# Optimization experiments

Measured on AMD Instinct MI355X. Metric: run time of the kernel, lower is better.

Reference implementation:

```python
import jax, jax.numpy as jnp
import numpy as np

TAU = 0.1          # temperature from init_kwargs
EPS = 1e-8         # torch.nn.CosineSimilarity default eps


def setup_inputs() -> dict:
    key = jax.random.key(0)
    k1, k2, k3 = jax.random.split(key, 3)
    B, D = 2048, 128
    return {
        "z_i": jax.random.normal(k1, (B, D), dtype=jnp.float32),
        "z_j": jax.random.normal(k2, (B, D), dtype=jnp.float32),
        "y": jax.random.randint(k3, (B,), 0, 10, dtype=jnp.int64),
    }


def reference(z_i, z_j, y):
    # p: (2N, D)
    p = jnp.concatenate([z_i, z_j], axis=0)
    n2 = p.shape[0]
    # Cosine similarity via norms + single GEMM (same math as pairwise
    # CosineSimilarity: dot / max(||a||*||b||, eps)), then temperature scale.
    norms = jnp.linalg.norm(p, axis=1)                      # (2N,)
    sim = (p @ p.T) / jnp.maximum(norms[:, None] * norms[None, :], EPS) / TAU

    # Positive mask: same label, diagonal removed.
    y2 = jnp.concatenate([y, y], axis=0)                    # (2N,)
    off_diag = 1.0 - jnp.eye(n2, dtype=sim.dtype)           # logit mask
    mask = (y2[:, None] == y2[None, :]).astype(sim.dtype) * off_diag

    # Masked log-softmax over each row (self excluded from denominator).
    exp_logits = jnp.exp(sim) * off_diag
    log_prob = sim - jnp.log(exp_logits.sum(axis=1, keepdims=True))

    mean_log_prob_pos = (mask * log_prob).sum(axis=1) / mask.sum(axis=1)
    return -mean_log_prob_pos.mean()
```

## Files before the change

kernel.cpp:

```cpp
#include <hip/hip_runtime.h>

#define N2 4096
#define D 128
#define TAU_INV 10.0f
#define E2SCALE 14.4269504088896340736f
#define BM 256
#define BN 256
#define NT (BN / 32)
#define NIT (N2 / BM)
#define GEMM_BLOCKS (NIT * NIT)
#define NCLS 10
#define CGRP 16
#define CROWS (N2 / CGRP)
#define CB (NCLS * CGRP)
#define PCW 130

typedef __attribute__((ext_vector_type(8))) short bf16x8;
typedef __attribute__((ext_vector_type(16))) float floatx16;

__device__ __forceinline__ short f2bf(float f) {
    unsigned u = __float_as_uint(f);
    u = (u + 0x7fff + ((u >> 16) & 1)) >> 16;
    return (short)u;
}
__device__ __forceinline__ float bf2f(short s) {
    return __uint_as_float(((unsigned)(unsigned short)s) << 16);
}

__global__ __launch_bounds__(512) void main_kernel(const float* __restrict__ zi,
                                                   const float* __restrict__ zj,
                                                   const long long* __restrict__ y,
                                                   float* __restrict__ pse,
                                                   float* __restrict__ pcls) {
    __shared__ short ldsB[BN * D];
    int tid = threadIdx.x;
    int wave = tid >> 6;
    int lane = tid & 63;

    if (blockIdx.x >= GEMM_BLOCKS) {
        float* shf = (float*)ldsB;
        int cb = blockIdx.x - GEMM_BLOCKS;
        int c  = cb / CGRP;
        int g  = cb % CGRP;

        float sSx = 0.f, sSy = 0.f, sT = 0.f, cnt = 0.f;
        for (int i = 0; i < CROWS / 8; ++i) {
            int r = g * CROWS + wave * (CROWS / 8) + i;
            const float* src = (r < 2048) ? (zi + r * D) : (zj + (r - 2048) * D);
            float2 v = ((const float2*)src)[lane];
            float ss = v.x * v.x + v.y * v.y;
            #pragma unroll
            for (int m = 1; m < 64; m <<= 1) ss += __shfl_xor(ss, m);
            float inv = 1.0f / sqrtf(ss);
            float qx = bf2f(f2bf(v.x * inv));
            float qy = bf2f(f2bf(v.y * inv));
            bool m = ((int)y[r & 2047] == c);
            sSx += m ? qx : 0.f;
            sSy += m ? qy : 0.f;
            sT  += m ? (qx * qx + qy * qy) : 0.f;
            cnt += m ? 1.f : 0.f;
        }
        shf[wave * D + 2 * lane]     = sSx;
        shf[wave * D + 2 * lane + 1] = sSy;
        #pragma unroll
        for (int m = 1; m < 64; m <<= 1) sT += __shfl_xor(sT, m);
        if (lane == 0) { shf[1024 + wave] = sT; shf[1032 + wave] = cnt; }
        __syncthreads();
        if (tid < D) {
            float s = 0.f;
            #pragma unroll
            for (int w = 0; w < 8; ++w) s += shf[w * D + tid];
            pcls[cb * PCW + tid] = s;
        } else if (tid == D) {
            float s = 0.f;
            #pragma unroll
            for (int w = 0; w < 8; ++w) s += shf[1024 + w];
            pcls[cb * PCW + 128] = s;
        } else if (tid == D + 1) {
            float s = 0.f;
            #pragma unroll
            for (int w = 0; w < 8; ++w) s += shf[1032 + w];
            pcls[cb * PCW + 129] = s;
        }
        return;
    }

    int gb = blockIdx.x;
    int col  = lane & 31;
    int half = lane >> 5;
    int it = gb >> 4;
    int js = gb & 15;
    int rbase = it * BM + wave * 32;

    #pragma unroll
    for (int pass = 0; pass < 2; ++pass) {
        int rl = pass * 128 + (tid >> 2);
        int q  = tid & 3;
        int gr = js * BN + rl;
        const float* srcb = (gr < 2048) ? (zi + gr * D) : (zj + (gr - 2048) * D);
        float4 b0[8];
        float part = 0.f;
        #pragma unroll
        for (int j = 0; j < 8; ++j) {
            float4 u = *(const float4*)(srcb + q * 32 + j * 4);
            part += u.x * u.x + u.y * u.y + u.z * u.z + u.w * u.w;
            b0[j] = u;
        }
        part += __shfl_xor(part, 1);
        part += __shfl_xor(part, 2);
        float invb = 1.0f / sqrtf(part);
        #pragma unroll
        for (int jj = 0; jj < 4; ++jj) {
            float4 u = b0[2 * jj], v = b0[2 * jj + 1];
            bf16x8 t;
            t[0] = f2bf(u.x * invb); t[1] = f2bf(u.y * invb);
            t[2] = f2bf(u.z * invb); t[3] = f2bf(u.w * invb);
            t[4] = f2bf(v.x * invb); t[5] = f2bf(v.y * invb);
            t[6] = f2bf(v.z * invb); t[7] = f2bf(v.w * invb);
            *(bf16x8*)&ldsB[(rl >> 5) * 4096 + (q * 4 + jj) * 256 + (rl & 31) * 8] = t;
        }
    }

    bf16x8 af[8];
    {
        int grow = rbase + col;
        const float* srca = (grow < 2048) ? (zi + grow * D) : (zj + (grow - 2048) * D);
        float4 a0[8], a1[8];
        float ssq = 0.f;
        #pragma unroll
        for (int k = 0; k < 8; ++k) {
            float4 u = *(const float4*)(srca + k * 16 + half * 8);
            float4 v = *(const float4*)(srca + k * 16 + half * 8 + 4);
            ssq += u.x * u.x + u.y * u.y + u.z * u.z + u.w * u.w
                 + v.x * v.x + v.y * v.y + v.z * v.z + v.w * v.w;
            a0[k] = u; a1[k] = v;
        }
        ssq += __shfl_xor(ssq, 32);
        float inv = 1.0f / sqrtf(ssq);
        #pragma unroll
        for (int k = 0; k < 8; ++k) {
            bf16x8 t;
            t[0] = f2bf(a0[k].x * inv); t[1] = f2bf(a0[k].y * inv);
            t[2] = f2bf(a0[k].z * inv); t[3] = f2bf(a0[k].w * inv);
            t[4] = f2bf(a1[k].x * inv); t[5] = f2bf(a1[k].y * inv);
            t[6] = f2bf(a1[k].z * inv); t[7] = f2bf(a1[k].w * inv);
            af[k] = t;
        }
    }

    float se[16];
    #pragma unroll
    for (int r = 0; r < 16; ++r) se[r] = 0.f;

    __syncthreads();

    const bf16x8* lb = (const bf16x8*)ldsB;
    #pragma unroll
    for (int t = 0; t < NT; ++t) {
        int j0 = js * BN + t * 32;

        floatx16 acc;
        #pragma unroll
        for (int r = 0; r < 16; ++r) acc[r] = 0.f;
        #pragma unroll
        for (int k = 0; k < 8; ++k)
            acc = __builtin_amdgcn_mfma_f32_32x32x16_bf16(
                af[k], lb[t * 512 + k * 64 + lane], acc, 0, 0, 0);

        if (j0 == rbase) {
            int jcol = j0 + col;
            #pragma unroll
            for (int r = 0; r < 16; ++r) {
                int rowr = rbase + (r & 3) + 8 * (r >> 2) + 4 * half;
                float e = __builtin_amdgcn_exp2f(acc[r] * E2SCALE);
                se[r] += (rowr == jcol) ? 0.f : e;
            }
        } else {
            #pragma unroll
            for (int r = 0; r < 16; ++r)
                se[r] += __builtin_amdgcn_exp2f(acc[r] * E2SCALE);
        }
    }

    #pragma unroll
    for (int r = 0; r < 16; ++r) {
        float a = se[r];
        #pragma unroll
        for (int m = 1; m < 32; m <<= 1) a += __shfl_xor(a, m);
        if (col == 0) {
            int rowr = rbase + (r & 3) + 8 * (r >> 2) + 4 * half;
            pse[rowr * NIT + js] = a;
        }
    }
}

__global__ __launch_bounds__(512) void finish_kernel(const float* __restrict__ pse,
                                                     const float* __restrict__ pcls,
                                                     float* __restrict__ out) {
    __shared__ float red[16];
    int tid = threadIdx.x;
    int wave = tid >> 6;
    int lane = tid & 63;

    float L = 0.f;
    for (int r = tid; r < N2; r += 512) {
        float s = 0.f;
        #pragma unroll
        for (int js = 0; js < NIT; ++js) s += pse[r * NIT + js];
        L += __logf(s);
    }
    #pragma unroll
    for (int m = 1; m < 64; m <<= 1) L += __shfl_xor(L, m);

    float P = 0.f;
    for (int c = wave; c < NCLS; c += 8) {
        float Sx = 0.f, Sy = 0.f, T = 0.f, n = 0.f;
        #pragma unroll
        for (int g = 0; g < CGRP; ++g) {
            const float* p = pcls + (c * CGRP + g) * PCW;
            Sx += p[2 * lane];
            Sy += p[2 * lane + 1];
            T  += p[128];
            n  += p[129];
        }
        float s2 = Sx * Sx + Sy * Sy;
        #pragma unroll
        for (int m = 1; m < 64; m <<= 1) s2 += __shfl_xor(s2, m);
        P += (n >= 2.0f) ? (s2 - T) * TAU_INV / (n - 1.0f) : 0.f;
    }

    if (lane == 0) { red[wave] = L; red[8 + wave] = P; }
    __syncthreads();
    if (tid == 0) {
        float Ls = 0.f, Ps = 0.f;
        #pragma unroll
        for (int w = 0; w < 8; ++w) { Ls += red[w]; Ps += red[8 + w]; }
        out[0] = (Ls - Ps) * (1.0f / (float)N2);
    }
}

extern "C" void kernel_launch(void* const* d_in, const int* in_sizes, int n_in,
                              void* d_out, int out_size, void* d_ws, size_t ws_size,
                              hipStream_t stream) {
    const float*     zi = (const float*)d_in[0];
    const float*     zj = (const float*)d_in[1];
    const long long* y  = (const long long*)d_in[2];
    float* out = (float*)d_out;

    char* ws = (char*)d_ws;
    float* pse  = (float*)ws;
    float* pcls = pse + N2 * NIT;

    main_kernel<<<GEMM_BLOCKS + CB, 512, 0, stream>>>(zi, zj, y, pse, pcls);
    finish_kernel<<<1, 512, 0, stream>>>(pse, pcls, out);
}
```

Measured before the change: 89.82 us.

## Fuse per-class sums into diagonal GEMM blocks using LDS-resident normalized tiles

Drops the 160 separate class-statistics blocks that re-read and re-normalized every row from global memory. The 16 diagonal GEMM blocks (it == js) now reuse their already normalized bf16 B tile in LDS to accumulate per-class vector sums, squared norms and counts with LDS atomics, writing one 1300-float partial per block. The finish kernel sums 16 partials instead of 160. The trade-off is extra serial work and LDS atomic contention on only 16 blocks, which may lengthen the critical path of those blocks.

```diff
diff --git a/kernel.cpp b/kernel.cpp
--- a/kernel.cpp
+++ b/kernel.cpp
@@ -10,10 +10,7 @@
 #define NIT (N2 / BM)
 #define GEMM_BLOCKS (NIT * NIT)
 #define NCLS 10
-#define CGRP 16
-#define CROWS (N2 / CGRP)
-#define CB (NCLS * CGRP)
-#define PCW 130
+#define PCB 1300
 
 typedef __attribute__((ext_vector_type(8))) short bf16x8;
 typedef __attribute__((ext_vector_type(16))) float floatx16;
@@ -33,58 +30,10 @@
                                                    float* __restrict__ pse,
                                                    float* __restrict__ pcls) {
     __shared__ short ldsB[BN * D];
+    __shared__ float shF[PCB + 12];
     int tid = threadIdx.x;
     int wave = tid >> 6;
     int lane = tid & 63;
-
-    if (blockIdx.x >= GEMM_BLOCKS) {
-        float* shf = (float*)ldsB;
-        int cb = blockIdx.x - GEMM_BLOCKS;
-        int c  = cb / CGRP;
-        int g  = cb % CGRP;
-
-        float sSx = 0.f, sSy = 0.f, sT = 0.f, cnt = 0.f;
-        for (int i = 0; i < CROWS / 8; ++i) {
-            int r = g * CROWS + wave * (CROWS / 8) + i;
-            const float* src = (r < 2048) ? (zi + r * D) : (zj + (r - 2048) * D);
-            float2 v = ((const float2*)src)[lane];
-            float ss = v.x * v.x + v.y * v.y;
-            #pragma unroll
-            for (int m = 1; m < 64; m <<= 1) ss += __shfl_xor(ss, m);
-            float inv = 1.0f / sqrtf(ss);
-            float qx = bf2f(f2bf(v.x * inv));
-            float qy = bf2f(f2bf(v.y * inv));
-            bool m = ((int)y[r & 2047] == c);
-            sSx += m ? qx : 0.f;
-            sSy += m ? qy : 0.f;
-            sT  += m ? (qx * qx + qy * qy) : 0.f;
-            cnt += m ? 1.f : 0.f;
-        }
-        shf[wave * D + 2 * lane]     = sSx;
-        shf[wave * D + 2 * lane + 1] = sSy;
-        #pragma unroll
-        for (int m = 1; m < 64; m <<= 1) sT += __shfl_xor(sT, m);
-        if (lane == 0) { shf[1024 + wave] = sT; shf[1032 + wave] = cnt; }
-        __syncthreads();
-        if (tid < D) {
-            float s = 0.f;
-            #pragma unroll
-            for (int w = 0; w < 8; ++w) s += shf[w * D + tid];
-            pcls[cb * PCW + tid] = s;
-        } else if (tid == D) {
-            float s = 0.f;
-            #pragma unroll
-            for (int w = 0; w < 8; ++w) s += shf[1024 + w];
-            pcls[cb * PCW + 128] = s;
-        } else if (tid == D + 1) {
-            float s = 0.f;
-            #pragma unroll
-            for (int w = 0; w < 8; ++w) s += shf[1032 + w];
-            pcls[cb * PCW + 129] = s;
-        }
-        return;
-    }
-
     int gb = blockIdx.x;
     int col  = lane & 31;
     int half = lane >> 5;
@@ -192,6 +141,34 @@
             pse[rowr * NIT + js] = a;
         }
     }
+
+    if (it == js) {
+        for (int k = tid; k < PCB; k += 512) shF[k] = 0.f;
+        __syncthreads();
+        int d0 = 4 * (tid & 31);
+        for (int i = 0; i < 16; ++i) {
+            int rl = (tid >> 5) + 16 * i;
+            int c = (int)y[(js * BN + rl) & 2047];
+            const short* p = &ldsB[(rl >> 5) * 4096 + (d0 >> 3) * 256 + (rl & 31) * 8 + (d0 & 7)];
+            float q0 = bf2f(p[0]), q1 = bf2f(p[1]), q2 = bf2f(p[2]), q3 = bf2f(p[3]);
+            bool ok = ((unsigned)c < (unsigned)NCLS);
+            if (ok) {
+                atomicAdd(&shF[c * D + d0],     q0);
+                atomicAdd(&shF[c * D + d0 + 1], q1);
+                atomicAdd(&shF[c * D + d0 + 2], q2);
+                atomicAdd(&shF[c * D + d0 + 3], q3);
+            }
+            float t4 = q0 * q0 + q1 * q1 + q2 * q2 + q3 * q3;
+            #pragma unroll
+            for (int m = 1; m < 32; m <<= 1) t4 += __shfl_xor(t4, m);
+            if ((tid & 31) == 0 && ok) {
+                atomicAdd(&shF[NCLS * D + c], t4);
+                atomicAdd(&shF[NCLS * D + NCLS + c], 1.f);
+            }
+        }
+        __syncthreads();
+        for (int k = tid; k < PCB; k += 512) pcls[it * PCB + k] = shF[k];
+    }
 }
 
 __global__ __launch_bounds__(512) void finish_kernel(const float* __restrict__ pse,
@@ -216,12 +193,12 @@
     for (int c = wave; c < NCLS; c += 8) {
         float Sx = 0.f, Sy = 0.f, T = 0.f, n = 0.f;
         #pragma unroll
-        for (int g = 0; g < CGRP; ++g) {
-            const float* p = pcls + (c * CGRP + g) * PCW;
-            Sx += p[2 * lane];
-            Sy += p[2 * lane + 1];
-            T  += p[128];
-            n  += p[129];
+        for (int b = 0; b < NIT; ++b) {
+            const float* p = pcls + b * PCB;
+            Sx += p[c * D + 2 * lane];
+            Sy += p[c * D + 2 * lane + 1];
+            T  += p[NCLS * D + c];
+            n  += p[NCLS * D + NCLS + c];
         }
         float s2 = Sx * Sx + Sy * Sy;
         #pragma unroll
@@ -251,6 +228,6 @@
     float* pse  = (float*)ws;
     float* pcls = pse + N2 * NIT;
 
-    main_kernel<<<GEMM_BLOCKS + CB, 512, 0, stream>>>(zi, zj, y, pse, pcls);
+    main_kernel<<<GEMM_BLOCKS, 512, 0, stream>>>(zi, zj, y, pse, pcls);
     finish_kernel<<<1, 512, 0, stream>>>(pse, pcls, out);
 }
```

New measurement: 126.4 us. 40.7% more time.
